# Optimization experiments

Hardware: AMD Instinct MI355X
Metric: run time of the kernel (lower is better)

Reference implementation:

```python
import math
import jax, jax.numpy as jnp
import numpy as np

B, N, D, H = 2, 8192, 1024, 16


def setup_inputs() -> dict:
    key = jax.random.key(0)
    k1, k2, k3, k4 = jax.random.split(key, 4)
    s = 1.0 / math.sqrt(D)
    return {
        "x": jax.random.normal(k1, (B, N, D), dtype=jnp.float32),
        "W_qk": jax.random.normal(k2, (D, D), dtype=jnp.float32) * s,
        "W_v": jax.random.normal(k3, (D, D), dtype=jnp.float32) * s,
        "W_out": jax.random.normal(k4, (D, D), dtype=jnp.float32) * s,
        "tau": jnp.ones((H, 1, 1), dtype=jnp.float32),
    }


def reference(x, W_qk, W_v, W_out, tau):
    b, n, d = x.shape
    h = H
    dh = d // h
    # QK / V projections (no bias), then to channel-major (B, H, dh, N)
    qk = (x @ W_qk).transpose(0, 2, 1).reshape(b, h, dh, n)
    v = (x @ W_v).transpose(0, 2, 1).reshape(b, h, dh, n)
    # Cross-channel Gram matrix over tokens: (B, H, dh, dh)
    dot = jnp.einsum('bhcn,bhdn->bhcd', qk, qk)
    q2 = jnp.sum(qk * qk, axis=-1)  # (B, H, dh)
    # Negative squared Euclidean distance between channel vectors
    logits = (2.0 * dot - q2[:, :, :, None] - q2[:, :, None, :]) / math.sqrt(max(n, 1))
    logits = logits * tau[None, ...]
    attn = jax.nn.softmax(logits, axis=-1)  # (B, H, dh, dh)
    w = jnp.einsum('bhcd,bhdn->bhcn', attn, v)  # (B, H, dh, N)
    out = w.reshape(b, d, n).transpose(0, 2, 1) @ W_out  # (B, N, D)
    return out
```

## Files before the change

kernel.cpp:

```cpp
#include <hip/hip_runtime.h>
#include <hip/hip_bf16.h>
#include <cstdint>
#include <cstddef>

typedef __bf16 v8bf __attribute__((ext_vector_type(8)));
typedef float  v4f  __attribute__((ext_vector_type(4)));

__device__ __forceinline__ unsigned short f2bf(float f) {
    unsigned int u = __float_as_uint(f);
    u += 0x7fffu + ((u >> 16) & 1u);
    return (unsigned short)(u >> 16);
}

__device__ __forceinline__ void gload_lds16(const unsigned short* g, unsigned short* l) {
    __builtin_amdgcn_global_load_lds(
        (const __attribute__((address_space(1))) unsigned int*)(uintptr_t)g,
        (__attribute__((address_space(3))) unsigned int*)(uintptr_t)l, 16, 0, 0);
}

template<int WRITE_BF16>
__global__ __launch_bounds__(256, 2) void gemm_bt(
    const unsigned short* __restrict__ A,
    const unsigned short* __restrict__ BT,
    void* __restrict__ C,
    int K, int lda, int ldb, int ldc,
    size_t sAz, size_t sBz, size_t sCz,
    int nBlk, int mPerXcd)
{
    __shared__ unsigned short sA[128 * 32];
    __shared__ unsigned short sB[128 * 32];

    const int id = blockIdx.x;
    const int xcd = id & 7;
    int s = id >> 3;
    const int perXcd = mPerXcd * nBlk;
    const int z = s / perXcd;
    s -= z * perXcd;
    const int mB = xcd * mPerXcd + s / nBlk;
    const int nB = s - (s / nBlk) * nBlk;

    const unsigned short* Ab = A + (size_t)z * sAz;
    const unsigned short* Bb = BT + (size_t)z * sBz;

    const int tid  = threadIdx.x;
    const int wv   = tid >> 6;
    const int lane = tid & 63;
    const int quad = lane >> 4;
    const int l16  = lane & 15;
    const size_t bm = (size_t)mB * 128;
    const size_t bn = (size_t)nB * 128;
    const int wm = (wv >> 1) * 64;
    const int wn = (wv & 1) * 64;

    const int ro = tid >> 2;
    const int ko = (((tid & 3) ^ (ro & 3)) << 3);

    const unsigned short* aptr0 = Ab + (bm + ro)      * (size_t)lda + ko;
    const unsigned short* aptr1 = Ab + (bm + ro + 64) * (size_t)lda + ko;
    const unsigned short* bptr0 = Bb + (bn + ro)      * (size_t)ldb + ko;
    const unsigned short* bptr1 = Bb + (bn + ro + 64) * (size_t)ldb + ko;

    unsigned short* sA0 = &sA[wv * 512];
    unsigned short* sA1 = &sA[2048 + wv * 512];
    unsigned short* sB0 = &sB[wv * 512];
    unsigned short* sB1 = &sB[2048 + wv * 512];

    const int sslot = ((quad ^ (l16 & 3)) << 3);

    v4f acc[4][4] = {};

    for (int k0 = 0; k0 < K; k0 += 32) {
        gload_lds16(aptr0 + k0, sA0);
        gload_lds16(aptr1 + k0, sA1);
        gload_lds16(bptr0 + k0, sB0);
        gload_lds16(bptr1 + k0, sB1);
        __syncthreads();

        v8bf af[4], bfr[4];
        #pragma unroll
        for (int t = 0; t < 4; t++) {
            af[t]  = *(const v8bf*)&sA[(size_t)(wm + t * 16 + l16) * 32 + sslot];
            bfr[t] = *(const v8bf*)&sB[(size_t)(wn + t * 16 + l16) * 32 + sslot];
        }

        #pragma unroll
        for (int ti = 0; ti < 4; ti++)
            #pragma unroll
            for (int tj = 0; tj < 4; tj++)
                acc[ti][tj] = __builtin_amdgcn_mfma_f32_16x16x32_bf16(
                    af[ti], bfr[tj], acc[ti][tj], 0, 0, 0);
        __syncthreads();
    }

    if (WRITE_BF16) {
        unsigned short* Cb = (unsigned short*)C + (size_t)z * sCz;
        #pragma unroll
        for (int ti = 0; ti < 4; ti++) {
            const size_t row0 = bm + wm + ti * 16 + quad * 4;
            #pragma unroll
            for (int tj = 0; tj < 4; tj++) {
                const size_t col = bn + wn + tj * 16 + l16;
                #pragma unroll
                for (int r = 0; r < 4; r++)
                    Cb[(row0 + r) * (size_t)ldc + col] = f2bf(acc[ti][tj][r]);
            }
        }
    } else {
        float* Cb = (float*)C + (size_t)z * sCz;
        #pragma unroll
        for (int ti = 0; ti < 4; ti++) {
            const size_t row0 = bm + wm + ti * 16 + quad * 4;
            #pragma unroll
            for (int tj = 0; tj < 4; tj++) {
                const size_t col = bn + wn + tj * 16 + l16;
                #pragma unroll
                for (int r = 0; r < 4; r++)
                    Cb[(row0 + r) * (size_t)ldc + col] = acc[ti][tj][r];
            }
        }
    }
}

#define MFMA_QUAD(MH, NH)                                                     \
    do {                                                                      \
        __builtin_amdgcn_s_setprio(1);                                        \
        _Pragma("unroll")                                                     \
        for (int mi = 0; mi < 4; ++mi) {                                      \
            _Pragma("unroll")                                                 \
            for (int ni = 0; ni < 2; ++ni) {                                  \
                acc[(MH)*4 + mi][(NH)*2 + ni] =                               \
                    __builtin_amdgcn_mfma_f32_16x16x32_bf16(                  \
                        aF[mi][0], bF[NH][ni][0],                             \
                        acc[(MH)*4 + mi][(NH)*2 + ni], 0, 0, 0);              \
                acc[(MH)*4 + mi][(NH)*2 + ni] =                               \
                    __builtin_amdgcn_mfma_f32_16x16x32_bf16(                  \
                        aF[mi][1], bF[NH][ni][1],                             \
                        acc[(MH)*4 + mi][(NH)*2 + ni], 0, 0, 0);              \
            }                                                                 \
        }                                                                     \
        __builtin_amdgcn_s_setprio(0);                                        \
    } while (0)

template<int WRITE_BF16>
__global__ __launch_bounds__(512, 2) void gemm256_bt(
    const unsigned short* __restrict__ A,
    const unsigned short* __restrict__ BT,
    void* __restrict__ C,
    int K, int lda, int ldb, int ldc,
    size_t sAz, size_t sBz, size_t sCz,
    int nBlk, int mPerXcd, int swapBig)
{
    __shared__ unsigned short sm[65536];

    const int id = blockIdx.x;
    const int xcd = id & 7;
    int s = id >> 3;
    const int perXcd = mPerXcd * nBlk;
    const int z = s / perXcd;
    s -= z * perXcd;
    const int bigB   = xcd * mPerXcd + s / nBlk;
    const int smallB = s - (s / nBlk) * nBlk;
    const int mB = swapBig ? smallB : bigB;
    const int nB = swapBig ? bigB : smallB;

    const unsigned short* Ab = A + (size_t)z * sAz;
    const unsigned short* Bb = BT + (size_t)z * sBz;

    const int tid  = threadIdx.x;
    const int wv   = tid >> 6;
    const int lane = tid & 63;
    const int quad = lane >> 4;
    const int l16  = lane & 15;
    const int wm   = wv >> 2;
    const int wn   = wv & 3;

    const size_t bm = (size_t)mB * 256;
    const size_t bn = (size_t)nB * 256;

    const int r0   = tid >> 3;
    const int slog = (tid & 7) ^ (r0 & 7);
    const unsigned short* aP = Ab + (bm + r0) * (size_t)lda + slog * 8;
    const unsigned short* bP = Bb + (bn + r0) * (size_t)ldb + slog * 8;

    const int stA = wv * 512;

    const int soff0 = (quad ^ (l16 & 7)) * 8;
    const int arow0 = (wm * 64 + l16) * 64 + soff0;
    const int brow0 = (wn * 32 + l16) * 64 + soff0;

    v4f  acc[8][4] = {};
    v8bf aF[4][2];
    v8bf bF[2][2][2];

    const int NT = K >> 6;

    {
        gload_lds16(aP,                sm + stA);
        gload_lds16(aP + 64 * lda,     sm + stA + 4096);
        gload_lds16(bP,                sm + 32768 + stA);
        gload_lds16(bP + 64 * ldb,     sm + 32768 + stA + 4096);
        gload_lds16(bP + 128 * ldb,    sm + 32768 + 8192 + stA);
        gload_lds16(bP + 192 * ldb,    sm + 32768 + 8192 + stA + 4096);
        gload_lds16(aP + 128 * lda,    sm + 8192 + stA);
        gload_lds16(aP + 192 * lda,    sm + 8192 + stA + 4096);
        if (NT > 1) {
            gload_lds16(aP + 64,                 sm + 16384 + stA);
            gload_lds16(aP + 64 * lda + 64,      sm + 16384 + stA + 4096);
            gload_lds16(bP + 64,                 sm + 32768 + 16384 + stA);
            gload_lds16(bP + 64 * ldb + 64,      sm + 32768 + 16384 + stA + 4096);
            gload_lds16(bP + 128 * ldb + 64,     sm + 32768 + 16384 + 8192 + stA);
            gload_lds16(bP + 192 * ldb + 64,     sm + 32768 + 16384 + 8192 + stA + 4096);
            asm volatile("s_waitcnt vmcnt(6)" ::: "memory");
        } else {
            asm volatile("s_waitcnt vmcnt(0)" ::: "memory");
        }
        __builtin_amdgcn_s_barrier();
    }

    for (int t = 0; t < NT; ++t) {
        const int p = t & 1;
        const unsigned short* sa = sm + p * 16384;
        const unsigned short* sb = sm + 32768 + p * 16384;
        unsigned short* dq = sm + (p ^ 1) * 16384;
        unsigned short* dp = sm + p * 16384;
        const int kk1 = (t + 1) * 64;
        const int kk2 = (t + 2) * 64;

        #pragma unroll
        for (int mi = 0; mi < 4; ++mi) {
            aF[mi][0] = *(const v8bf*)(sa + (arow0 + mi * 1024));
            aF[mi][1] = *(const v8bf*)(sa + ((arow0 + mi * 1024) ^ 32));
        }
        #pragma unroll
        for (int ni = 0; ni < 2; ++ni) {
            bF[0][ni][0] = *(const v8bf*)(sb + (brow0 + ni * 1024));
            bF[0][ni][1] = *(const v8bf*)(sb + ((brow0 + ni * 1024) ^ 32));
        }
        if (t + 1 < NT) {
            gload_lds16(aP + 128 * lda + kk1, dq + 8192 + stA);
            gload_lds16(aP + 192 * lda + kk1, dq + 8192 + stA + 4096);
        }
        __builtin_amdgcn_s_barrier();
        asm volatile("s_waitcnt lgkmcnt(0)" ::: "memory");
        MFMA_QUAD(0, 0);
        __builtin_amdgcn_s_barrier();

        #pragma unroll
        for (int ni = 0; ni < 2; ++ni) {
            bF[1][ni][0] = *(const v8bf*)(sb + 8192 + (brow0 + ni * 1024));
            bF[1][ni][1] = *(const v8bf*)(sb + 8192 + ((brow0 + ni * 1024) ^ 32));
        }
        if (t + 2 < NT) {
            gload_lds16(aP + kk2,            dp + stA);
            gload_lds16(aP + 64 * lda + kk2, dp + stA + 4096);
        }
        __builtin_amdgcn_s_barrier();
        asm volatile("s_waitcnt lgkmcnt(0)" ::: "memory");
        MFMA_QUAD(0, 1);
        __builtin_amdgcn_s_barrier();

        #pragma unroll
        for (int mi = 0; mi < 4; ++mi) {
            aF[mi][0] = *(const v8bf*)(sa + 8192 + (arow0 + mi * 1024));
            aF[mi][1] = *(const v8bf*)(sa + 8192 + ((arow0 + mi * 1024) ^ 32));
        }
        if (t + 2 < NT) {
            gload_lds16(bP + kk2,            dp + 32768 + stA);
            gload_lds16(bP + 64 * ldb + kk2, dp + 32768 + stA + 4096);
        }
        __builtin_amdgcn_s_barrier();
        asm volatile("s_waitcnt lgkmcnt(0)" ::: "memory");
        MFMA_QUAD(1, 1);
        __builtin_amdgcn_s_barrier();

        if (t + 2 < NT) {
            gload_lds16(bP + 128 * ldb + kk2, dp + 32768 + 8192 + stA);
            gload_lds16(bP + 192 * ldb + kk2, dp + 32768 + 8192 + stA + 4096);
            asm volatile("s_waitcnt vmcnt(6)" ::: "memory");
        } else {
            asm volatile("s_waitcnt vmcnt(0)" ::: "memory");
        }
        __builtin_amdgcn_s_barrier();
        MFMA_QUAD(1, 0);
        __builtin_amdgcn_s_barrier();
    }

    if (WRITE_BF16) {
        unsigned short* Cb = (unsigned short*)C + (size_t)z * sCz;
        #pragma unroll
        for (int mh = 0; mh < 2; ++mh)
            #pragma unroll
            for (int mi = 0; mi < 4; ++mi) {
                const size_t row0 = bm + mh * 128 + wm * 64 + mi * 16 + quad * 4;
                #pragma unroll
                for (int nh = 0; nh < 2; ++nh)
                    #pragma unroll
                    for (int ni = 0; ni < 2; ++ni) {
                        const size_t col = bn + nh * 128 + wn * 32 + ni * 16 + l16;
                        #pragma unroll
                        for (int r = 0; r < 4; ++r)
                            Cb[(row0 + r) * (size_t)ldc + col] =
                                f2bf(acc[mh * 4 + mi][nh * 2 + ni][r]);
                    }
            }
    } else {
        float* Cb = (float*)C + (size_t)z * sCz;
        #pragma unroll
        for (int mh = 0; mh < 2; ++mh)
            #pragma unroll
            for (int mi = 0; mi < 4; ++mi) {
                const size_t row0 = bm + mh * 128 + wm * 64 + mi * 16 + quad * 4;
                #pragma unroll
                for (int nh = 0; nh < 2; ++nh)
                    #pragma unroll
                    for (int ni = 0; ni < 2; ++ni) {
                        const size_t col = bn + nh * 128 + wn * 32 + ni * 16 + l16;
                        #pragma unroll
                        for (int r = 0; r < 4; ++r)
                            Cb[(row0 + r) * (size_t)ldc + col] =
                                acc[mh * 4 + mi][nh * 2 + ni][r];
                    }
            }
    }
}
#undef MFMA_QUAD

__global__ __launch_bounds__(256, 2) void gram_kernel(
    const unsigned short* __restrict__ qkT,
    float* __restrict__ partial)
{
    const int bh = blockIdx.x;
    const int split = blockIdx.y;
    const int b = bh >> 4, h = bh & 15;
    const unsigned short* base =
        qkT + (size_t)(h * 64) * 16384 + (size_t)b * 8192 + (size_t)split * 512;

    __shared__ unsigned short sM[64 * 512];
    const int tid = threadIdx.x;
    const int wv = tid >> 6, lane = tid & 63, quad = lane >> 4, l16 = lane & 15;

    #pragma unroll
    for (int i = 0; i < 16; i++) {
        const int row = i * 4 + wv;
        const int lo  = (lane & 56) | ((lane & 7) ^ (row & 7));
        gload_lds16(base + (size_t)row * 16384 + lo * 8,
                    sM + (size_t)i * 2048 + wv * 512);
    }
    __syncthreads();

    v4f acc[4] = {};
    const int cha = 16 * wv + l16;

    #pragma unroll
    for (int ks = 0; ks < 16; ks++) {
        const int lg = ks * 4 + quad;
        const int so = ((lg & 56) | ((lg & 7) ^ (l16 & 7))) * 8;
        const v8bf a = *(const v8bf*)&sM[(size_t)cha * 512 + so];
        #pragma unroll
        for (int t = 0; t < 4; t++) {
            const v8bf bb = *(const v8bf*)&sM[(size_t)(t * 16 + l16) * 512 + so];
            acc[t] = __builtin_amdgcn_mfma_f32_16x16x32_bf16(a, bb, acc[t], 0, 0, 0);
        }
    }

    float* outp = partial + ((size_t)split * 32 + bh) * 4096;
    #pragma unroll
    for (int t = 0; t < 4; t++)
        #pragma unroll
        for (int r = 0; r < 4; r++)
            outp[(size_t)(16 * wv + quad * 4 + r) * 64 + t * 16 + l16] = acc[t][r];
}

__global__ __launch_bounds__(256) void softmax_kernel(
    const float* __restrict__ partial,
    const float* __restrict__ tau,
    float* __restrict__ attnT)
{
    const int gw = (int)((blockIdx.x * 256 + threadIdx.x) >> 6);
    const int d = threadIdx.x & 63;
    const int bh = gw >> 6;
    const int c = gw & 63;
    const int h = bh & 15;

    float cd = 0.f, cc = 0.f, dd = 0.f;
    #pragma unroll
    for (int s = 0; s < 16; s++) {
        const float* p = partial + ((size_t)s * 32 + bh) * 4096;
        cd += p[c * 64 + d];
        cc += p[c * 65];
        dd += p[d * 65];
    }
    const float INV_SQRT_N = 0.011048543456039806f;
    const float logit = (2.f * cd - cc - dd) * INV_SQRT_N * tau[h];

    float m = logit;
    #pragma unroll
    for (int off = 32; off > 0; off >>= 1) m = fmaxf(m, __shfl_xor(m, off, 64));
    const float e = __expf(logit - m);
    float sum = e;
    #pragma unroll
    for (int off = 32; off > 0; off >>= 1) sum += __shfl_xor(sum, off, 64);

    attnT[(size_t)bh * 4096 + d * 64 + c] = e / sum;
}

__global__ __launch_bounds__(256) void wefft_kernel(
    const float* __restrict__ attnT,
    const float* __restrict__ Wout,
    unsigned short* __restrict__ weffT)
{
    const int bh = blockIdx.x;
    const int jg = blockIdx.y;
    const int b = bh >> 4, h = bh & 15;

    __shared__ float sAttT[64][65];
    __shared__ float sW[64][65];
    const int tid = threadIdx.x;
    const float* ap = attnT + (size_t)bh * 4096;
    const float* wp = Wout + (size_t)(h * 64) * 1024 + jg * 64;
    for (int i = tid; i < 4096; i += 256) {
        const int r = i >> 6, q = i & 63;
        sAttT[r][q] = ap[i];
        sW[r][q] = wp[(size_t)r * 1024 + q];
    }
    __syncthreads();

    const int dd0 = (tid >> 4) << 2;
    const int j0  = (tid & 15) << 2;
    float acc[4][4] = {};
    for (int cc = 0; cc < 64; cc++) {
        float av[4], wvv[4];
        #pragma unroll
        for (int i = 0; i < 4; i++) av[i] = sAttT[dd0 + i][cc];
        #pragma unroll
        for (int i = 0; i < 4; i++) wvv[i] = sW[cc][j0 + i];
        #pragma unroll
        for (int i = 0; i < 4; i++)
            #pragma unroll
            for (int j = 0; j < 4; j++)
                acc[i][j] += av[i] * wvv[j];
    }

    unsigned short* op = weffT + ((size_t)b * 1024 + jg * 64) * 1024 + h * 64;
    #pragma unroll
    for (int i = 0; i < 4; i++)
        #pragma unroll
        for (int j = 0; j < 4; j++)
            op[(size_t)(j0 + j) * 1024 + dd0 + i] = f2bf(acc[i][j]);
}

__global__ __launch_bounds__(256) void cvt_all_kernel(
    const float* __restrict__ x, const float* __restrict__ Wv,
    const float* __restrict__ Wqk,
    unsigned short* __restrict__ xb, unsigned short* __restrict__ wvb,
    unsigned short* __restrict__ wqkT)
{
    const int bid = blockIdx.x;
    if (bid < 17408) {
        const float* src = (bid < 16384) ? x : Wv;
        unsigned short* dst = (bid < 16384) ? xb : wvb;
        const size_t blk = (bid < 16384) ? bid : (bid - 16384);
        const size_t i = (blk * 256 + threadIdx.x) * 4;
        const float4 v = *(const float4*)(src + i);
        ushort4 o;
        o.x = f2bf(v.x); o.y = f2bf(v.y); o.z = f2bf(v.z); o.w = f2bf(v.w);
        *(ushort4*)(dst + i) = o;
    } else {
        const int t = bid - 17408;
        const int n0 = (t & 31) * 32, k0 = (t >> 5) * 32;
        __shared__ float sT[32][33];
        const int tx = threadIdx.x & 31, ty = threadIdx.x >> 5;
        #pragma unroll
        for (int i = ty; i < 32; i += 8)
            sT[i][tx] = Wqk[(size_t)(k0 + i) * 1024 + n0 + tx];
        __syncthreads();
        #pragma unroll
        for (int i = ty; i < 32; i += 8)
            wqkT[(size_t)(n0 + i) * 1024 + k0 + tx] = f2bf(sT[tx][i]);
    }
}

extern "C" void kernel_launch(void* const* d_in, const int* in_sizes, int n_in,
                              void* d_out, int out_size, void* d_ws, size_t ws_size,
                              hipStream_t stream)
{
    (void)in_sizes; (void)n_in; (void)out_size; (void)ws_size;
    const float* x    = (const float*)d_in[0];
    const float* Wqk  = (const float*)d_in[1];
    const float* Wv   = (const float*)d_in[2];
    const float* Wout = (const float*)d_in[3];
    const float* tau  = (const float*)d_in[4];

    unsigned short* xb     = (unsigned short*)d_ws;
    unsigned short* wqkT   = xb + (size_t)16384 * 1024;
    unsigned short* wvb    = wqkT + (size_t)1024 * 1024;
    unsigned short* qkT    = wvb + (size_t)1024 * 1024;
    float*          partial= (float*)(qkT + (size_t)16384 * 1024);
    float*          attnT  = partial + (size_t)16 * 32 * 4096;
    unsigned short* weffT  = (unsigned short*)(attnT + (size_t)32 * 4096);
    unsigned short* wfoldT = weffT + (size_t)2 * 1024 * 1024;

    cvt_all_kernel<<<18432, 256, 0, stream>>>(x, Wv, Wqk, xb, wvb, wqkT);

    gemm256_bt<1><<<256, 512, 0, stream>>>(
        wqkT, xb, (void*)qkT, 1024, 1024, 1024, 16384, 0, 0, 0, 4, 8, 1);

    gram_kernel<<<dim3(32, 16), 256, 0, stream>>>(qkT, partial);
    softmax_kernel<<<512, 256, 0, stream>>>(partial, tau, attnT);
    wefft_kernel<<<dim3(32, 16), 256, 0, stream>>>(attnT, Wout, weffT);

    gemm_bt<1><<<128, 256, 0, stream>>>(
        weffT, wvb, (void*)wfoldT, 1024, 1024, 1024, 1024,
        (size_t)1024 * 1024, 0, (size_t)1024 * 1024, 8, 1);

    gemm256_bt<0><<<256, 512, 0, stream>>>(
        xb, wfoldT, d_out, 1024, 1024, 1024, 1024,
        (size_t)8192 * 1024, (size_t)1024 * 1024, (size_t)8192 * 1024, 4, 4, 0);
}
```

Before: 253.0 us.

## Restructure 256x256 GEMM main loop into two phases with fewer barriers

The four-phase inner loop of the 256-tile bf16 GEMM becomes two phases. Each phase runs two MFMA quadrants back to back and loads both B fragment halves at once. Global-to-LDS prefetches for the next-next tile are grouped into one batch, and the vmcnt waits are retuned. This halves the barriers per K-step and lengthens uninterrupted MFMA runs, in exchange for more live B-fragment registers and altered wait counts, which risks races or spills.

```diff
diff --git a/kernel.cpp b/kernel.cpp
--- a/kernel.cpp
+++ b/kernel.cpp
@@ -121,7 +121,7 @@
     }
 }
 
-#define MFMA_QUAD(MH, NH)                                                     \
+#define MFMA_Q(MH, NH, BF)                                                    \
     do {                                                                      \
         __builtin_amdgcn_s_setprio(1);                                        \
         _Pragma("unroll")                                                     \
@@ -130,11 +130,11 @@
             for (int ni = 0; ni < 2; ++ni) {                                  \
                 acc[(MH)*4 + mi][(NH)*2 + ni] =                               \
                     __builtin_amdgcn_mfma_f32_16x16x32_bf16(                  \
-                        aF[mi][0], bF[NH][ni][0],                             \
+                        aF[mi][0], BF[ni][0],                                 \
                         acc[(MH)*4 + mi][(NH)*2 + ni], 0, 0, 0);              \
                 acc[(MH)*4 + mi][(NH)*2 + ni] =                               \
                     __builtin_amdgcn_mfma_f32_16x16x32_bf16(                  \
-                        aF[mi][1], bF[NH][ni][1],                             \
+                        aF[mi][1], BF[ni][1],                                 \
                         acc[(MH)*4 + mi][(NH)*2 + ni], 0, 0, 0);              \
             }                                                                 \
         }                                                                     \
@@ -190,7 +190,8 @@
 
     v4f  acc[8][4] = {};
     v8bf aF[4][2];
-    v8bf bF[2][2][2];
+    v8bf b0[2][2];
+    v8bf b1[2][2];
 
     const int NT = K >> 6;
 
@@ -210,7 +211,7 @@
             gload_lds16(bP + 64 * ldb + 64,      sm + 32768 + 16384 + stA + 4096);
             gload_lds16(bP + 128 * ldb + 64,     sm + 32768 + 16384 + 8192 + stA);
             gload_lds16(bP + 192 * ldb + 64,     sm + 32768 + 16384 + 8192 + stA + 4096);
-            asm volatile("s_waitcnt vmcnt(6)" ::: "memory");
+            asm volatile("s_waitcnt vmcnt(8)" ::: "memory");
         } else {
             asm volatile("s_waitcnt vmcnt(0)" ::: "memory");
         }
@@ -233,30 +234,22 @@
         }
         #pragma unroll
         for (int ni = 0; ni < 2; ++ni) {
-            bF[0][ni][0] = *(const v8bf*)(sb + (brow0 + ni * 1024));
-            bF[0][ni][1] = *(const v8bf*)(sb + ((brow0 + ni * 1024) ^ 32));
+            b0[ni][0] = *(const v8bf*)(sb + (brow0 + ni * 1024));
+            b0[ni][1] = *(const v8bf*)(sb + ((brow0 + ni * 1024) ^ 32));
+            b1[ni][0] = *(const v8bf*)(sb + 8192 + (brow0 + ni * 1024));
+            b1[ni][1] = *(const v8bf*)(sb + 8192 + ((brow0 + ni * 1024) ^ 32));
         }
         if (t + 1 < NT) {
             gload_lds16(aP + 128 * lda + kk1, dq + 8192 + stA);
             gload_lds16(aP + 192 * lda + kk1, dq + 8192 + stA + 4096);
+            asm volatile("s_waitcnt vmcnt(8)" ::: "memory");
+        } else {
+            asm volatile("s_waitcnt vmcnt(0)" ::: "memory");
         }
         __builtin_amdgcn_s_barrier();
         asm volatile("s_waitcnt lgkmcnt(0)" ::: "memory");
-        MFMA_QUAD(0, 0);
-        __builtin_amdgcn_s_barrier();
-
-        #pragma unroll
-        for (int ni = 0; ni < 2; ++ni) {
-            bF[1][ni][0] = *(const v8bf*)(sb + 8192 + (brow0 + ni * 1024));
-            bF[1][ni][1] = *(const v8bf*)(sb + 8192 + ((brow0 + ni * 1024) ^ 32));
-        }
-        if (t + 2 < NT) {
-            gload_lds16(aP + kk2,            dp + stA);
-            gload_lds16(aP + 64 * lda + kk2, dp + stA + 4096);
-        }
-        __builtin_amdgcn_s_barrier();
-        asm volatile("s_waitcnt lgkmcnt(0)" ::: "memory");
-        MFMA_QUAD(0, 1);
+        MFMA_Q(0, 0, b0);
+        MFMA_Q(0, 1, b1);
         __builtin_amdgcn_s_barrier();
 
         #pragma unroll
@@ -265,23 +258,20 @@
             aF[mi][1] = *(const v8bf*)(sa + 8192 + ((arow0 + mi * 1024) ^ 32));
         }
         if (t + 2 < NT) {
-            gload_lds16(bP + kk2,            dp + 32768 + stA);
-            gload_lds16(bP + 64 * ldb + kk2, dp + 32768 + stA + 4096);
+            gload_lds16(aP + kk2,             dp + stA);
+            gload_lds16(aP + 64 * lda + kk2,  dp + stA + 4096);
+            gload_lds16(bP + kk2,             dp + 32768 + stA);
+            gload_lds16(bP + 64 * ldb + kk2,  dp + 32768 + stA + 4096);
+            gload_lds16(bP + 128 * ldb + kk2, dp + 32768 + 8192 + stA);
+            gload_lds16(bP + 192 * ldb + kk2, dp + 32768 + 8192 + stA + 4096);
+            asm volatile("s_waitcnt vmcnt(8)" ::: "memory");
+        } else {
+            asm volatile("s_waitcnt vmcnt(2)" ::: "memory");
         }
         __builtin_amdgcn_s_barrier();
         asm volatile("s_waitcnt lgkmcnt(0)" ::: "memory");
-        MFMA_QUAD(1, 1);
-        __builtin_amdgcn_s_barrier();
-
-        if (t + 2 < NT) {
-            gload_lds16(bP + 128 * ldb + kk2, dp + 32768 + 8192 + stA);
-            gload_lds16(bP + 192 * ldb + kk2, dp + 32768 + 8192 + stA + 4096);
-            asm volatile("s_waitcnt vmcnt(6)" ::: "memory");
-        } else {
-            asm volatile("s_waitcnt vmcnt(0)" ::: "memory");
-        }
-        __builtin_amdgcn_s_barrier();
-        MFMA_QUAD(1, 0);
+        MFMA_Q(1, 1, b1);
+        MFMA_Q(1, 0, b0);
         __builtin_amdgcn_s_barrier();
     }
 
@@ -323,7 +313,7 @@
             }
     }
 }
-#undef MFMA_QUAD
+#undef MFMA_Q
 
 __global__ __launch_bounds__(256, 2) void gram_kernel(
     const unsigned short* __restrict__ qkT,
```

Result: no change. 254.9 us (+0.8%).

## Fuse split-K reduction and softmax into the attn-times-Wout kernel

Applied to the files above, without the earlier changes.

Merges the softmax kernel and the attnT·W_out kernel into one kernel. Each block reduces the 16 split partials for one (b,h), computes the row softmax in shared memory, then loops over 4 output column groups of W_out. This removes one launch and the round trip of attnT through global memory. The cost is that each block redundantly recomputes the reduction and softmax, four times per bh across the grid, and the grid drops to 128 blocks with a serial loop inside each.

```diff
diff --git a/kernel.cpp b/kernel.cpp
--- a/kernel.cpp
+++ b/kernel.cpp
@@ -371,82 +371,97 @@
             outp[(size_t)(16 * wv + quad * 4 + r) * 64 + t * 16 + l16] = acc[t][r];
 }
 
-__global__ __launch_bounds__(256) void softmax_kernel(
+__global__ __launch_bounds__(256) void smw_kernel(
     const float* __restrict__ partial,
     const float* __restrict__ tau,
-    float* __restrict__ attnT)
-{
-    const int gw = (int)((blockIdx.x * 256 + threadIdx.x) >> 6);
-    const int d = threadIdx.x & 63;
-    const int bh = gw >> 6;
-    const int c = gw & 63;
-    const int h = bh & 15;
-
-    float cd = 0.f, cc = 0.f, dd = 0.f;
-    #pragma unroll
-    for (int s = 0; s < 16; s++) {
-        const float* p = partial + ((size_t)s * 32 + bh) * 4096;
-        cd += p[c * 64 + d];
-        cc += p[c * 65];
-        dd += p[d * 65];
-    }
-    const float INV_SQRT_N = 0.011048543456039806f;
-    const float logit = (2.f * cd - cc - dd) * INV_SQRT_N * tau[h];
-
-    float m = logit;
-    #pragma unroll
-    for (int off = 32; off > 0; off >>= 1) m = fmaxf(m, __shfl_xor(m, off, 64));
-    const float e = __expf(logit - m);
-    float sum = e;
-    #pragma unroll
-    for (int off = 32; off > 0; off >>= 1) sum += __shfl_xor(sum, off, 64);
-
-    attnT[(size_t)bh * 4096 + d * 64 + c] = e / sum;
-}
-
-__global__ __launch_bounds__(256) void wefft_kernel(
-    const float* __restrict__ attnT,
     const float* __restrict__ Wout,
     unsigned short* __restrict__ weffT)
 {
     const int bh = blockIdx.x;
-    const int jg = blockIdx.y;
+    const int jq = blockIdx.y;
     const int b = bh >> 4, h = bh & 15;
-
-    __shared__ float sAttT[64][65];
+    const int tid = threadIdx.x;
+
+    __shared__ float sattn[64][65];
+    __shared__ float sdiag[64];
     __shared__ float sW[64][65];
-    const int tid = threadIdx.x;
-    const float* ap = attnT + (size_t)bh * 4096;
-    const float* wp = Wout + (size_t)(h * 64) * 1024 + jg * 64;
-    for (int i = tid; i < 4096; i += 256) {
-        const int r = i >> 6, q = i & 63;
-        sAttT[r][q] = ap[i];
-        sW[r][q] = wp[(size_t)r * 1024 + q];
-    }
+
+    float dacc[16];
+    #pragma unroll
+    for (int k = 0; k < 16; k++) dacc[k] = 0.f;
+    const float* pb = partial + (size_t)bh * 4096;
+    for (int s = 0; s < 16; s++) {
+        const float* p = pb + (size_t)s * 32 * 4096;
+        #pragma unroll
+        for (int k = 0; k < 16; k++) dacc[k] += p[k * 256 + tid];
+    }
+    #pragma unroll
+    for (int k = 0; k < 16; k++) {
+        const int idx = k * 256 + tid;
+        sattn[idx >> 6][idx & 63] = dacc[k];
+    }
+    __syncthreads();
+    if (tid < 64) sdiag[tid] = sattn[tid][tid];
+    __syncthreads();
+
+    const int c   = tid >> 2;
+    const int sub = tid & 3;
+    const float tauh = tau[h];
+    const float INV_SQRT_N = 0.011048543456039806f;
+    float lg[16];
+    float m = -3.4e38f;
+    #pragma unroll
+    for (int q = 0; q < 16; q++) {
+        const int d = sub * 16 + q;
+        lg[q] = (2.f * sattn[c][d] - sdiag[c] - sdiag[d]) * INV_SQRT_N * tauh;
+        m = fmaxf(m, lg[q]);
+    }
+    m = fmaxf(m, __shfl_xor(m, 1, 64));
+    m = fmaxf(m, __shfl_xor(m, 2, 64));
+    float sum = 0.f;
+    #pragma unroll
+    for (int q = 0; q < 16; q++) { lg[q] = __expf(lg[q] - m); sum += lg[q]; }
+    sum += __shfl_xor(sum, 1, 64);
+    sum += __shfl_xor(sum, 2, 64);
+    const float inv = 1.f / sum;
+    __syncthreads();
+    #pragma unroll
+    for (int q = 0; q < 16; q++)
+        sattn[sub * 16 + q][c] = lg[q] * inv;
     __syncthreads();
 
     const int dd0 = (tid >> 4) << 2;
     const int j0  = (tid & 15) << 2;
-    float acc[4][4] = {};
-    for (int cc = 0; cc < 64; cc++) {
-        float av[4], wvv[4];
-        #pragma unroll
-        for (int i = 0; i < 4; i++) av[i] = sAttT[dd0 + i][cc];
-        #pragma unroll
-        for (int i = 0; i < 4; i++) wvv[i] = sW[cc][j0 + i];
+    for (int jg = jq * 4; jg < jq * 4 + 4; ++jg) {
+        const float* wp = Wout + (size_t)(h * 64) * 1024 + jg * 64;
+        for (int i = tid; i < 4096; i += 256) {
+            const int r = i >> 6, q = i & 63;
+            sW[r][q] = wp[(size_t)r * 1024 + q];
+        }
+        __syncthreads();
+
+        float acc[4][4] = {};
+        for (int cc = 0; cc < 64; cc++) {
+            float av[4], wv4[4];
+            #pragma unroll
+            for (int i = 0; i < 4; i++) av[i] = sattn[dd0 + i][cc];
+            #pragma unroll
+            for (int i = 0; i < 4; i++) wv4[i] = sW[cc][j0 + i];
+            #pragma unroll
+            for (int i = 0; i < 4; i++)
+                #pragma unroll
+                for (int j = 0; j < 4; j++)
+                    acc[i][j] += av[i] * wv4[j];
+        }
+
+        unsigned short* op = weffT + ((size_t)b * 1024 + jg * 64) * 1024 + h * 64;
         #pragma unroll
         for (int i = 0; i < 4; i++)
             #pragma unroll
             for (int j = 0; j < 4; j++)
-                acc[i][j] += av[i] * wvv[j];
-    }
-
-    unsigned short* op = weffT + ((size_t)b * 1024 + jg * 64) * 1024 + h * 64;
-    #pragma unroll
-    for (int i = 0; i < 4; i++)
-        #pragma unroll
-        for (int j = 0; j < 4; j++)
-            op[(size_t)(j0 + j) * 1024 + dd0 + i] = f2bf(acc[i][j]);
+                op[(size_t)(j0 + j) * 1024 + dd0 + i] = f2bf(acc[i][j]);
+        __syncthreads();
+    }
 }
 
 __global__ __launch_bounds__(256) void cvt_all_kernel(
@@ -506,8 +521,8 @@
         wqkT, xb, (void*)qkT, 1024, 1024, 1024, 16384, 0, 0, 0, 4, 8, 1);
 
     gram_kernel<<<dim3(32, 16), 256, 0, stream>>>(qkT, partial);
-    softmax_kernel<<<512, 256, 0, stream>>>(partial, tau, attnT);
-    wefft_kernel<<<dim3(32, 16), 256, 0, stream>>>(attnT, Wout, weffT);
+
+    smw_kernel<<<dim3(32, 4), 256, 0, stream>>>(partial, tau, Wout, weffT);
 
     gemm_bt<1><<<128, 256, 0, stream>>>(
         weffT, wvb, (void*)wfoldT, 1024, 1024, 1024, 1024,
```

After: 270.4 us. 6.9% more time.
